# Kernel tuning notes

Hardware: AMD Instinct MI355X
Metric: run time of the kernel (lower is better)

Reference implementation:

```python
import jax, jax.numpy as jnp
import numpy as np

B, S, D = 8, 2048, 256
H, DFF, L = 8, 1024, 5
DK = D // H
EPS = 1e-5


def _xavier(key, shape):
    fan_in, fan_out = shape[-2], shape[-1]
    a = jnp.sqrt(6.0 / (fan_in + fan_out))
    return jax.random.uniform(key, shape, jnp.float32, -a, a)


def setup_inputs() -> dict:
    key = jax.random.key(0)
    ks = jax.random.split(key, 12)
    inp = {
        "src": jax.random.normal(ks[0], (B, S, D), jnp.float32),
        "sph": jax.random.normal(ks[1], (B, S, S), jnp.float32),
        # stacked per-layer parameters, leading dim = L
        "Wq": _xavier(ks[2], (L, D, D)), "bq": jnp.zeros((L, D), jnp.float32),
        "Wk": _xavier(ks[3], (L, D, D)), "bk": jnp.zeros((L, D), jnp.float32),
        "Wv": _xavier(ks[4], (L, D, D)), "bv": jnp.zeros((L, D), jnp.float32),
        "Wo": _xavier(ks[5], (L, D, D)), "bo": jnp.zeros((L, D), jnp.float32),
        "W1": _xavier(ks[6], (L, D, DFF)), "b1": jnp.zeros((L, DFF), jnp.float32),
        "W2": _xavier(ks[7], (L, DFF, D)), "b2": jnp.zeros((L, D), jnp.float32),
        "ln1_g": jnp.ones((L, D), jnp.float32), "ln1_b": jnp.zeros((L, D), jnp.float32),
        "ln2_g": jnp.ones((L, D), jnp.float32), "ln2_b": jnp.zeros((L, D), jnp.float32),
    }
    return inp


def _layernorm(x, g, b):
    mu = jnp.mean(x, axis=-1, keepdims=True)
    var = jnp.mean(jnp.square(x - mu), axis=-1, keepdims=True)
    return (x - mu) * jax.lax.rsqrt(var + EPS) * g + b


def _layer(x, sph, Wq, bq, Wk, bk, Wv, bv, Wo, bo, W1, b1, W2, b2, g1, be1, g2, be2):
    # multihead attention with additive sph score bias
    q = (x @ Wq + bq).reshape(B, S, H, DK)
    k = (x @ Wk + bk).reshape(B, S, H, DK)
    v = (x @ Wv + bv).reshape(B, S, H, DK)
    scores = jnp.einsum("bqhd,bkhd->bhqk", q, k) / jnp.sqrt(jnp.float32(DK))
    scores = scores + sph[:, None, :, :]  # bias broadcast over heads
    attn = jax.nn.softmax(scores, axis=-1)
    ctx = jnp.einsum("bhqk,bkhd->bqhd", attn, v).reshape(B, S, D)
    src2 = ctx @ Wo + bo
    x = _layernorm(x + src2, g1, be1)
    # FFN (exact gelu, matching torch F.gelu default)
    h = jax.nn.gelu(x @ W1 + b1, approximate=False)
    src2 = h @ W2 + b2
    x = _layernorm(x + src2, g2, be2)
    return x


def reference(src, sph, Wq, bq, Wk, bk, Wv, bv, Wo, bo, W1, b1, W2, b2, ln1_g, ln1_b, ln2_g, ln2_b):
    x = src
    for i in range(L):
        x = _layer(x, sph, Wq[i], bq[i], Wk[i], bk[i], Wv[i], bv[i], Wo[i], bo[i],
                   W1[i], b1[i], W2[i], b2[i], ln1_g[i], ln1_b[i], ln2_g[i], ln2_b[i])
    return x
```

## Files before the change

### kernel.cpp

```cpp
#include <hip/hip_runtime.h>
#include <cstdint>

__device__ __forceinline__ float b2f(unsigned short u) {
    unsigned int t = ((unsigned int)u) << 16;
    float f;
    __builtin_memcpy(&f, &t, 4);
    return f;
}
__device__ __forceinline__ unsigned short f2b(float f) {
    unsigned int u;
    __builtin_memcpy(&u, &f, 4);
    unsigned int r = (u + 0x7FFFu + ((u >> 16) & 1u)) >> 16;
    return (unsigned short)r;
}
__device__ __forceinline__ float2 bpair(unsigned int u) {
    float2 r;
    unsigned int lo = u << 16;
    unsigned int hi = u & 0xFFFF0000u;
    __builtin_memcpy(&r.x, &lo, 4);
    __builtin_memcpy(&r.y, &hi, 4);
    return r;
}

typedef __attribute__((ext_vector_type(8))) short bf16x8;
typedef __attribute__((ext_vector_type(4))) float f32x4;

#define LOG2E 1.4426950408889634f
#define SC2   0.2550348595f

__global__ void transcvt_k(const float* __restrict__ in,
                           unsigned short* __restrict__ out, int R, int C,
                           int in_z, int out_z) {
    __shared__ float tile[32][33];
    in += (size_t)blockIdx.z * in_z;
    out += (size_t)blockIdx.z * out_z;
    const int c0 = blockIdx.x * 32, r0 = blockIdx.y * 32;
    const int tx = threadIdx.x, ty = threadIdx.y;
#pragma unroll
    for (int i = 0; i < 32; i += 8)
        tile[ty + i][tx] = in[(size_t)(r0 + ty + i) * C + c0 + tx];
    __syncthreads();
#pragma unroll
    for (int i = 0; i < 32; i += 8)
        out[(size_t)(c0 + ty + i) * R + r0 + tx] = f2b(tile[tx][ty + i]);
}

__global__ __launch_bounds__(256) void sph_cvt(const float* __restrict__ in,
                                               unsigned short* __restrict__ out) {
    const size_t idx = (size_t)blockIdx.x * 256 + threadIdx.x;
    const float4 a = ((const float4*)in)[idx * 2];
    const float4 b = ((const float4*)in)[idx * 2 + 1];
    uint4 o;
    o.x = (unsigned)f2b(a.x * LOG2E) | ((unsigned)f2b(a.y * LOG2E) << 16);
    o.y = (unsigned)f2b(a.z * LOG2E) | ((unsigned)f2b(a.w * LOG2E) << 16);
    o.z = (unsigned)f2b(b.x * LOG2E) | ((unsigned)f2b(b.y * LOG2E) << 16);
    o.w = (unsigned)f2b(b.z * LOG2E) | ((unsigned)f2b(b.w * LOG2E) << 16);
    ((uint4*)out)[idx] = o;
}

template <int AF32, int QKVB>
__global__ __launch_bounds__(256) void gemm_bias_kernel(
    const void* __restrict__ Ap, const unsigned short* __restrict__ Wt,
    const float* __restrict__ biasQ, const float* __restrict__ biasK,
    const float* __restrict__ biasV, unsigned short* __restrict__ C,
    int M, int N, int K, int do_gelu) {
    __shared__ unsigned short As[64 * 40];
    __shared__ unsigned short Bs[64 * 40];
    const int tid = threadIdx.x;
    const int lane = tid & 63, wid = tid >> 6;
    const int m0 = blockIdx.y * 64, n0 = blockIdx.x * 64;
    const int wm = (wid >> 1) * 32, wn = (wid & 1) * 32;
    const int quad = lane >> 4, mrow = lane & 15;
    f32x4 acc[2][2] = {};
    const int arow = tid >> 2, ak = (tid & 3) << 3;
    const unsigned short* Bg = Wt + (size_t)(n0 + arow) * K + ak;
    const float* Agf = (const float*)Ap + (size_t)(m0 + arow) * K + ak;
    const unsigned short* Agb = (const unsigned short*)Ap + (size_t)(m0 + arow) * K + ak;

    typedef __attribute__((ext_vector_type(8))) short short8;
    for (int kb = 0; kb < K; kb += 32) {
        if (AF32) {
            float4 f0 = *(const float4*)(Agf + kb);
            float4 f1 = *(const float4*)(Agf + kb + 4);
            short8 t;
            t[0] = (short)f2b(f0.x); t[1] = (short)f2b(f0.y);
            t[2] = (short)f2b(f0.z); t[3] = (short)f2b(f0.w);
            t[4] = (short)f2b(f1.x); t[5] = (short)f2b(f1.y);
            t[6] = (short)f2b(f1.z); t[7] = (short)f2b(f1.w);
            *(short8*)&As[arow * 40 + ak] = t;
        } else {
            *(uint4*)&As[arow * 40 + ak] = *(const uint4*)(Agb + kb);
        }
        *(uint4*)&Bs[arow * 40 + ak] = *(const uint4*)(Bg + kb);
        __syncthreads();
        bf16x8 a0 = *(const bf16x8*)&As[(wm + mrow) * 40 + quad * 8];
        bf16x8 a1 = *(const bf16x8*)&As[(wm + 16 + mrow) * 40 + quad * 8];
        bf16x8 b0 = *(const bf16x8*)&Bs[(wn + mrow) * 40 + quad * 8];
        bf16x8 b1 = *(const bf16x8*)&Bs[(wn + 16 + mrow) * 40 + quad * 8];
        acc[0][0] = __builtin_amdgcn_mfma_f32_16x16x32_bf16(a0, b0, acc[0][0], 0, 0, 0);
        acc[0][1] = __builtin_amdgcn_mfma_f32_16x16x32_bf16(a0, b1, acc[0][1], 0, 0, 0);
        acc[1][0] = __builtin_amdgcn_mfma_f32_16x16x32_bf16(a1, b0, acc[1][0], 0, 0, 0);
        acc[1][1] = __builtin_amdgcn_mfma_f32_16x16x32_bf16(a1, b1, acc[1][1], 0, 0, 0);
        __syncthreads();
    }
    const float* bp;
    if (QKVB) {
        const int bsel = n0 >> 8;
        bp = bsel == 0 ? biasQ : (bsel == 1 ? biasK : biasV);
    } else {
        bp = biasQ;
    }
#pragma unroll
    for (int i = 0; i < 2; i++)
#pragma unroll
        for (int j = 0; j < 2; j++) {
            const int col = n0 + wn + j * 16 + mrow;
            const float bv = QKVB ? bp[col & 255] : bp[col];
#pragma unroll
            for (int r = 0; r < 4; r++) {
                const int row = m0 + wm + i * 16 + quad * 4 + r;
                float v = acc[i][j][r] + bv;
                if (do_gelu) v = 0.5f * v * (1.0f + erff(v * 0.70710678118654752f));
                C[(size_t)row * N + col] = f2b(v);
            }
        }
}

template <int SPHB16>
__global__ __launch_bounds__(256) void attn_mfma(
    const unsigned short* __restrict__ Qb, const unsigned short* __restrict__ Kb,
    const unsigned short* __restrict__ Vb, const float* __restrict__ sphf,
    const unsigned short* __restrict__ sphb, unsigned short* __restrict__ Ctx) {
    __shared__ unsigned short Ks[64 * 40];
    __shared__ unsigned short Vt[32 * 72];
    __shared__ unsigned short Ps[4][16 * 72];

    const int tid = threadIdx.x, lane = tid & 63, wid = tid >> 6;
    const int quad = lane >> 4, lq = lane & 15;
    const int bid = blockIdx.x;
    const int h = bid >> 8, b = (bid >> 5) & 7, qt = bid & 31;
    const int q0 = qt * 64;
    const size_t bS = (size_t)b * 2048;

    const int skey = tid >> 2, sdg = (tid & 3) << 3;
    const unsigned short* kgp = Kb + (bS + skey) * 768 + h * 32 + sdg;
    const int vkp = tid & 31, vdg = (tid >> 5) << 2;
    const unsigned short* vgp = Vb + (bS + 2 * vkp) * 768 + h * 32 + vdg;

    const bf16x8 qf = *(const bf16x8*)(Qb + (bS + q0 + wid * 16 + lq) * 768 + h * 32 + quad * 8);

    const size_t sprow = ((size_t)b * 2048 + q0 + wid * 16 + quad * 4) * 2048 + lq;
    const float* spf = sphf + sprow;
    const unsigned short* spb = sphb + sprow;

    float l_r[4] = {0.f, 0.f, 0.f, 0.f};
    f32x4 o0 = {}, o1 = {};

    for (int kt = 0; kt < 32; ++kt) {
        const int k0 = kt * 64;
        __syncthreads();
        *(uint4*)&Ks[skey * 40 + sdg] = *(const uint4*)(kgp + (size_t)k0 * 768);
        {
            uint2 va = *(const uint2*)(vgp + (size_t)k0 * 768);
            uint2 vb2 = *(const uint2*)(vgp + (size_t)k0 * 768 + 768);
            *(unsigned int*)&Vt[(vdg + 0) * 72 + 2 * vkp] = (va.x & 0xFFFFu) | (vb2.x << 16);
            *(unsigned int*)&Vt[(vdg + 1) * 72 + 2 * vkp] = (va.x >> 16) | (vb2.x & 0xFFFF0000u);
            *(unsigned int*)&Vt[(vdg + 2) * 72 + 2 * vkp] = (va.y & 0xFFFFu) | (vb2.y << 16);
            *(unsigned int*)&Vt[(vdg + 3) * 72 + 2 * vkp] = (va.y >> 16) | (vb2.y & 0xFFFF0000u);
        }
        __syncthreads();

        const f32x4 zf = {};
        f32x4 sa0 = __builtin_amdgcn_mfma_f32_16x16x32_bf16(
            qf, *(const bf16x8*)&Ks[(0  + lq) * 40 + quad * 8], zf, 0, 0, 0);
        f32x4 sa1 = __builtin_amdgcn_mfma_f32_16x16x32_bf16(
            qf, *(const bf16x8*)&Ks[(16 + lq) * 40 + quad * 8], zf, 0, 0, 0);
        f32x4 sa2 = __builtin_amdgcn_mfma_f32_16x16x32_bf16(
            qf, *(const bf16x8*)&Ks[(32 + lq) * 40 + quad * 8], zf, 0, 0, 0);
        f32x4 sa3 = __builtin_amdgcn_mfma_f32_16x16x32_bf16(
            qf, *(const bf16x8*)&Ks[(48 + lq) * 40 + quad * 8], zf, 0, 0, 0);

#pragma unroll
        for (int r = 0; r < 4; ++r) {
            float sb0, sb1, sb2, sb3;
            if (SPHB16) {
                const unsigned short* spr = spb + (size_t)r * 2048 + k0;
                sb0 = b2f(spr[0]);  sb1 = b2f(spr[16]);
                sb2 = b2f(spr[32]); sb3 = b2f(spr[48]);
            } else {
                const float* spr = spf + (size_t)r * 2048 + k0;
                sb0 = spr[0]  * LOG2E; sb1 = spr[16] * LOG2E;
                sb2 = spr[32] * LOG2E; sb3 = spr[48] * LOG2E;
            }
            const float p0 = __builtin_amdgcn_exp2f(fmaf(sa0[r], SC2, sb0));
            const float p1 = __builtin_amdgcn_exp2f(fmaf(sa1[r], SC2, sb1));
            const float p2 = __builtin_amdgcn_exp2f(fmaf(sa2[r], SC2, sb2));
            const float p3 = __builtin_amdgcn_exp2f(fmaf(sa3[r], SC2, sb3));
            l_r[r] += (p0 + p1) + (p2 + p3);
            unsigned short* pw = &Ps[wid][(quad * 4 + r) * 72 + lq];
            pw[0]  = f2b(p0);
            pw[16] = f2b(p1);
            pw[32] = f2b(p2);
            pw[48] = f2b(p3);
        }

#pragma unroll
        for (int k2 = 0; k2 < 2; ++k2) {
            bf16x8 pf = *(const bf16x8*)&Ps[wid][lq * 72 + k2 * 32 + quad * 8];
            o0 = __builtin_amdgcn_mfma_f32_16x16x32_bf16(
                pf, *(const bf16x8*)&Vt[(0  + lq) * 72 + k2 * 32 + quad * 8], o0, 0, 0, 0);
            o1 = __builtin_amdgcn_mfma_f32_16x16x32_bf16(
                pf, *(const bf16x8*)&Vt[(16 + lq) * 72 + k2 * 32 + quad * 8], o1, 0, 0, 0);
        }
    }

    unsigned short* op = Ctx + (bS + q0 + wid * 16 + quad * 4) * 256 + h * 32;
#pragma unroll
    for (int r = 0; r < 4; ++r) {
        float l = l_r[r];
        l += __shfl_xor(l, 1);
        l += __shfl_xor(l, 2);
        l += __shfl_xor(l, 4);
        l += __shfl_xor(l, 8);
        const float inv = 1.f / l;
        op[r * 256 + lq]      = f2b(o0[r] * inv);
        op[r * 256 + 16 + lq] = f2b(o1[r] * inv);
    }
}

__global__ __launch_bounds__(256) void add_ln_kernel(
    const float* __restrict__ x, const unsigned short* __restrict__ r,
    const float* __restrict__ g, const float* __restrict__ be,
    float* __restrict__ out) {
    const int lane = threadIdx.x & 63, wid = threadIdx.x >> 6;
    const size_t row = (size_t)blockIdx.x * 4 + wid;
    float4 xv = *(const float4*)(x + row * 256 + lane * 4);
    uint2 ru = *(const uint2*)(r + row * 256 + lane * 4);
    float2 ra = bpair(ru.x), rb = bpair(ru.y);
    float v[4] = {xv.x + ra.x, xv.y + ra.y, xv.z + rb.x, xv.w + rb.y};
    float sum = v[0] + v[1] + v[2] + v[3];
#pragma unroll
    for (int off = 32; off; off >>= 1) sum += __shfl_xor(sum, off);
    const float mu = sum * (1.f / 256.f);
    float sq = 0.f;
#pragma unroll
    for (int i = 0; i < 4; i++) { float d = v[i] - mu; sq += d * d; }
#pragma unroll
    for (int off = 32; off; off >>= 1) sq += __shfl_xor(sq, off);
    const float rs = rsqrtf(sq * (1.f / 256.f) + 1e-5f);
    float4 o;
    o.x = (v[0] - mu) * rs * g[lane * 4 + 0] + be[lane * 4 + 0];
    o.y = (v[1] - mu) * rs * g[lane * 4 + 1] + be[lane * 4 + 1];
    o.z = (v[2] - mu) * rs * g[lane * 4 + 2] + be[lane * 4 + 2];
    o.w = (v[3] - mu) * rs * g[lane * 4 + 3] + be[lane * 4 + 3];
    *(float4*)(out + row * 256 + lane * 4) = o;
}

extern "C" void kernel_launch(void* const* d_in, const int* in_sizes, int n_in,
                              void* d_out, int out_size, void* d_ws, size_t ws_size,
                              hipStream_t stream) {
    const float* src = (const float*)d_in[0];
    const float* sph = (const float*)d_in[1];
    const float* Wq  = (const float*)d_in[2];
    const float* bq  = (const float*)d_in[3];
    const float* Wk  = (const float*)d_in[4];
    const float* bk  = (const float*)d_in[5];
    const float* Wv  = (const float*)d_in[6];
    const float* bv  = (const float*)d_in[7];
    const float* Wo  = (const float*)d_in[8];
    const float* bo  = (const float*)d_in[9];
    const float* W1  = (const float*)d_in[10];
    const float* b1  = (const float*)d_in[11];
    const float* W2  = (const float*)d_in[12];
    const float* b2  = (const float*)d_in[13];
    const float* g1  = (const float*)d_in[14];
    const float* be1 = (const float*)d_in[15];
    const float* g2  = (const float*)d_in[16];
    const float* be2 = (const float*)d_in[17];

    char* ws = (char*)d_ws;
    float* X = (float*)d_out;
    unsigned short* QKV = (unsigned short*)(ws + 0);
    unsigned short* CTX = (unsigned short*)(ws + 25165824);
    unsigned short* T2  = (unsigned short*)(ws + 33554432);
    unsigned short* H   = QKV;
    unsigned short* WtQKV = (unsigned short*)(ws + 41943040);
    unsigned short* WtO   = (unsigned short*)(ws + 43909120);
    unsigned short* Wt1   = (unsigned short*)(ws + 44564480);
    unsigned short* Wt2   = (unsigned short*)(ws + 47185920);
    unsigned short* SPHB  = (unsigned short*)(ws + 50331648);
    const int use_b16 = (ws_size >= (size_t)117440512);

    const dim3 tb(32, 8);
    transcvt_k<<<dim3(8, 8, 5),  tb, 0, stream>>>(Wq, WtQKV,          256, 256, 65536, 196608);
    transcvt_k<<<dim3(8, 8, 5),  tb, 0, stream>>>(Wk, WtQKV + 65536,  256, 256, 65536, 196608);
    transcvt_k<<<dim3(8, 8, 5),  tb, 0, stream>>>(Wv, WtQKV + 131072, 256, 256, 65536, 196608);
    transcvt_k<<<dim3(8, 8, 5),  tb, 0, stream>>>(Wo, WtO,            256, 256, 65536, 65536);
    transcvt_k<<<dim3(32, 8, 5), tb, 0, stream>>>(W1, Wt1,            256, 1024, 262144, 262144);
    transcvt_k<<<dim3(8, 32, 5), tb, 0, stream>>>(W2, Wt2,            1024, 256, 262144, 262144);
    if (use_b16) sph_cvt<<<16384, 256, 0, stream>>>(sph, SPHB);

    hipMemcpyAsync(X, src, 16777216, hipMemcpyDeviceToDevice, stream);

    const int M = 16384;
    for (int lyr = 0; lyr < 5; ++lyr) {
        gemm_bias_kernel<1, 1><<<dim3(12, 256), 256, 0, stream>>>(
            X, WtQKV + lyr * 196608, bq + lyr * 256, bk + lyr * 256, bv + lyr * 256,
            QKV, M, 768, 256, 0);
        if (use_b16)
            attn_mfma<1><<<2048, 256, 0, stream>>>(QKV, QKV + 256, QKV + 512, sph, SPHB, CTX);
        else
            attn_mfma<0><<<2048, 256, 0, stream>>>(QKV, QKV + 256, QKV + 512, sph, SPHB, CTX);
        gemm_bias_kernel<0, 0><<<dim3(4, 256), 256, 0, stream>>>(
            CTX, WtO + lyr * 65536, bo + lyr * 256, nullptr, nullptr, T2, M, 256, 256, 0);
        add_ln_kernel<<<4096, 256, 0, stream>>>(X, T2, g1 + lyr * 256, be1 + lyr * 256, X);
        gemm_bias_kernel<1, 0><<<dim3(16, 256), 256, 0, stream>>>(
            X, Wt1 + lyr * 262144, b1 + lyr * 1024, nullptr, nullptr, H, M, 1024, 256, 1);
        gemm_bias_kernel<0, 0><<<dim3(4, 256), 256, 0, stream>>>(
            H, Wt2 + lyr * 262144, b2 + lyr * 256, nullptr, nullptr, T2, M, 256, 1024, 0);
        add_ln_kernel<<<4096, 256, 0, stream>>>(X, T2, g2 + lyr * 256, be2 + lyr * 256, X);
    }
}
```

Baseline: 1.540 ms.

## Keep attention probabilities in registers by transposing score MFMA and permuting V layout

The score MFMA operands are swapped so each lane holds four consecutive keys for one query. The probabilities are then packed with v_cvt_pk_bf16_f32 straight into the A-operand of the PV MFMA, which removes the per-wave LDS P buffer and its store/load round trip. V rows are written to LDS in a permuted key order so they match the register-resident P layout. Bias loads become vectorized float4/uint2 reads, and the row-sum reduction is reworked to match the new lane mapping. The cost is a more fragile layout mapping whose correctness depends on the MFMA register permutation being exactly right.

```diff
diff --git a/kernel.cpp b/kernel.cpp
--- a/kernel.cpp
+++ b/kernel.cpp
@@ -21,9 +21,20 @@
     __builtin_memcpy(&r.y, &hi, 4);
     return r;
 }
+__device__ __forceinline__ unsigned int cvtpk(float lo, float hi) {
+    unsigned int r;
+    asm("v_cvt_pk_bf16_f32 %0, %1, %2" : "=v"(r) : "v"(lo), "v"(hi));
+    return r;
+}
 
 typedef __attribute__((ext_vector_type(8))) short bf16x8;
 typedef __attribute__((ext_vector_type(4))) float f32x4;
+
+__device__ __forceinline__ bf16x8 pack4(unsigned a, unsigned b, unsigned c, unsigned d) {
+    union { uint4 u; bf16x8 v; } x;
+    x.u = (uint4){a, b, c, d};
+    return x.v;
+}
 
 #define LOG2E 1.4426950408889634f
 #define SC2   0.2550348595f
@@ -133,7 +144,6 @@
     const unsigned short* __restrict__ sphb, unsigned short* __restrict__ Ctx) {
     __shared__ unsigned short Ks[64 * 40];
     __shared__ unsigned short Vt[32 * 72];
-    __shared__ unsigned short Ps[4][16 * 72];
 
     const int tid = threadIdx.x, lane = tid & 63, wid = tid >> 6;
     const int quad = lane >> 4, lq = lane & 15;
@@ -146,15 +156,18 @@
     const unsigned short* kgp = Kb + (bS + skey) * 768 + h * 32 + sdg;
     const int vkp = tid & 31, vdg = (tid >> 5) << 2;
     const unsigned short* vgp = Vb + (bS + 2 * vkp) * 768 + h * 32 + vdg;
+    const int vk2 = 2 * vkp;
+    const int vslot = (vk2 & 0x23) | ((vk2 & 0x0C) << 1) | ((vk2 & 0x10) >> 2);
 
     const bf16x8 qf = *(const bf16x8*)(Qb + (bS + q0 + wid * 16 + lq) * 768 + h * 32 + quad * 8);
 
-    const size_t sprow = ((size_t)b * 2048 + q0 + wid * 16 + quad * 4) * 2048 + lq;
-    const float* spf = sphf + sprow;
-    const unsigned short* spb = sphb + sprow;
-
-    float l_r[4] = {0.f, 0.f, 0.f, 0.f};
+    const size_t sbase = ((size_t)b * 2048 + q0 + wid * 16 + lq) * 2048 + 4 * quad;
+    const float* spf_ = sphf + sbase;
+    const unsigned short* spb_ = sphb + sbase;
+
+    float l_lane = 0.f;
     f32x4 o0 = {}, o1 = {};
+    const f32x4 zf = {};
 
     for (int kt = 0; kt < 32; ++kt) {
         const int k0 = kt * 64;
@@ -163,68 +176,58 @@
         {
             uint2 va = *(const uint2*)(vgp + (size_t)k0 * 768);
             uint2 vb2 = *(const uint2*)(vgp + (size_t)k0 * 768 + 768);
-            *(unsigned int*)&Vt[(vdg + 0) * 72 + 2 * vkp] = (va.x & 0xFFFFu) | (vb2.x << 16);
-            *(unsigned int*)&Vt[(vdg + 1) * 72 + 2 * vkp] = (va.x >> 16) | (vb2.x & 0xFFFF0000u);
-            *(unsigned int*)&Vt[(vdg + 2) * 72 + 2 * vkp] = (va.y & 0xFFFFu) | (vb2.y << 16);
-            *(unsigned int*)&Vt[(vdg + 3) * 72 + 2 * vkp] = (va.y >> 16) | (vb2.y & 0xFFFF0000u);
+            *(unsigned int*)&Vt[(vdg + 0) * 72 + vslot] = (va.x & 0xFFFFu) | (vb2.x << 16);
+            *(unsigned int*)&Vt[(vdg + 1) * 72 + vslot] = (va.x >> 16) | (vb2.x & 0xFFFF0000u);
+            *(unsigned int*)&Vt[(vdg + 2) * 72 + vslot] = (va.y & 0xFFFFu) | (vb2.y << 16);
+            *(unsigned int*)&Vt[(vdg + 3) * 72 + vslot] = (va.y >> 16) | (vb2.y & 0xFFFF0000u);
         }
         __syncthreads();
 
-        const f32x4 zf = {};
-        f32x4 sa0 = __builtin_amdgcn_mfma_f32_16x16x32_bf16(
-            qf, *(const bf16x8*)&Ks[(0  + lq) * 40 + quad * 8], zf, 0, 0, 0);
-        f32x4 sa1 = __builtin_amdgcn_mfma_f32_16x16x32_bf16(
-            qf, *(const bf16x8*)&Ks[(16 + lq) * 40 + quad * 8], zf, 0, 0, 0);
-        f32x4 sa2 = __builtin_amdgcn_mfma_f32_16x16x32_bf16(
-            qf, *(const bf16x8*)&Ks[(32 + lq) * 40 + quad * 8], zf, 0, 0, 0);
-        f32x4 sa3 = __builtin_amdgcn_mfma_f32_16x16x32_bf16(
-            qf, *(const bf16x8*)&Ks[(48 + lq) * 40 + quad * 8], zf, 0, 0, 0);
-
-#pragma unroll
-        for (int r = 0; r < 4; ++r) {
+        unsigned int w[4][2];
+#pragma unroll
+        for (int g = 0; g < 4; ++g) {
+            const bf16x8 kf = *(const bf16x8*)&Ks[(16 * g + lq) * 40 + quad * 8];
+            const f32x4 s = __builtin_amdgcn_mfma_f32_16x16x32_bf16(kf, qf, zf, 0, 0, 0);
             float sb0, sb1, sb2, sb3;
             if (SPHB16) {
-                const unsigned short* spr = spb + (size_t)r * 2048 + k0;
-                sb0 = b2f(spr[0]);  sb1 = b2f(spr[16]);
-                sb2 = b2f(spr[32]); sb3 = b2f(spr[48]);
+                const uint2 su = *(const uint2*)(spb_ + k0 + 16 * g);
+                const float2 lo = bpair(su.x), hi = bpair(su.y);
+                sb0 = lo.x; sb1 = lo.y; sb2 = hi.x; sb3 = hi.y;
             } else {
-                const float* spr = spf + (size_t)r * 2048 + k0;
-                sb0 = spr[0]  * LOG2E; sb1 = spr[16] * LOG2E;
-                sb2 = spr[32] * LOG2E; sb3 = spr[48] * LOG2E;
+                const float4 sf = *(const float4*)(spf_ + k0 + 16 * g);
+                sb0 = sf.x * LOG2E; sb1 = sf.y * LOG2E;
+                sb2 = sf.z * LOG2E; sb3 = sf.w * LOG2E;
             }
-            const float p0 = __builtin_amdgcn_exp2f(fmaf(sa0[r], SC2, sb0));
-            const float p1 = __builtin_amdgcn_exp2f(fmaf(sa1[r], SC2, sb1));
-            const float p2 = __builtin_amdgcn_exp2f(fmaf(sa2[r], SC2, sb2));
-            const float p3 = __builtin_amdgcn_exp2f(fmaf(sa3[r], SC2, sb3));
-            l_r[r] += (p0 + p1) + (p2 + p3);
-            unsigned short* pw = &Ps[wid][(quad * 4 + r) * 72 + lq];
-            pw[0]  = f2b(p0);
-            pw[16] = f2b(p1);
-            pw[32] = f2b(p2);
-            pw[48] = f2b(p3);
+            const float p0 = __builtin_amdgcn_exp2f(fmaf(s[0], SC2, sb0));
+            const float p1 = __builtin_amdgcn_exp2f(fmaf(s[1], SC2, sb1));
+            const float p2 = __builtin_amdgcn_exp2f(fmaf(s[2], SC2, sb2));
+            const float p3 = __builtin_amdgcn_exp2f(fmaf(s[3], SC2, sb3));
+            l_lane += (p0 + p1) + (p2 + p3);
+            w[g][0] = cvtpk(p0, p1);
+            w[g][1] = cvtpk(p2, p3);
         }
 
-#pragma unroll
-        for (int k2 = 0; k2 < 2; ++k2) {
-            bf16x8 pf = *(const bf16x8*)&Ps[wid][lq * 72 + k2 * 32 + quad * 8];
-            o0 = __builtin_amdgcn_mfma_f32_16x16x32_bf16(
-                pf, *(const bf16x8*)&Vt[(0  + lq) * 72 + k2 * 32 + quad * 8], o0, 0, 0, 0);
-            o1 = __builtin_amdgcn_mfma_f32_16x16x32_bf16(
-                pf, *(const bf16x8*)&Vt[(16 + lq) * 72 + k2 * 32 + quad * 8], o1, 0, 0, 0);
-        }
-    }
-
+        const bf16x8 pf0 = pack4(w[0][0], w[0][1], w[1][0], w[1][1]);
+        const bf16x8 pf1 = pack4(w[2][0], w[2][1], w[3][0], w[3][1]);
+        o0 = __builtin_amdgcn_mfma_f32_16x16x32_bf16(
+            pf0, *(const bf16x8*)&Vt[(0  + lq) * 72 + 0 * 32 + quad * 8], o0, 0, 0, 0);
+        o1 = __builtin_amdgcn_mfma_f32_16x16x32_bf16(
+            pf0, *(const bf16x8*)&Vt[(16 + lq) * 72 + 0 * 32 + quad * 8], o1, 0, 0, 0);
+        o0 = __builtin_amdgcn_mfma_f32_16x16x32_bf16(
+            pf1, *(const bf16x8*)&Vt[(0  + lq) * 72 + 1 * 32 + quad * 8], o0, 0, 0, 0);
+        o1 = __builtin_amdgcn_mfma_f32_16x16x32_bf16(
+            pf1, *(const bf16x8*)&Vt[(16 + lq) * 72 + 1 * 32 + quad * 8], o1, 0, 0, 0);
+    }
+
+    l_lane += __shfl_xor(l_lane, 16);
+    l_lane += __shfl_xor(l_lane, 32);
+    const float inv = 1.f / l_lane;
     unsigned short* op = Ctx + (bS + q0 + wid * 16 + quad * 4) * 256 + h * 32;
 #pragma unroll
     for (int r = 0; r < 4; ++r) {
-        float l = l_r[r];
-        l += __shfl_xor(l, 1);
-        l += __shfl_xor(l, 2);
-        l += __shfl_xor(l, 4);
-        l += __shfl_xor(l, 8);
-        const float inv = 1.f / l;
-        op[r * 256 + lq]      = f2b(o0[r] * inv);
-        op[r * 256 + 16 + lq] = f2b(o1[r] * inv);
+        const float ir = __shfl(inv, quad * 4 + r);
+        op[r * 256 + lq]      = f2b(o0[r] * ir);
+        op[r * 256 + 16 + lq] = f2b(o1[r] * ir);
     }
 }
 
```

Measured after the change: 1.786 ms. +16.0%, slower.

## Use 128-row GEMM tiles and emit bf16 activations from layernorm

Applied to the files above, without the earlier changes.

Adds a GEMM kernel with 128xTN block tiles, so each warp computes a 64-row slab with more MFMAs per shared-memory load. The layernorm kernel now also writes a bf16 copy of its output, so the QKV and FFN1 GEMMs read bf16 directly instead of converting fp32 activations inside the GEMM. The new path needs a larger workspace and falls back to the old kernels otherwise. Fewer blocks and more accumulator registers per thread may lower occupancy.

```diff
diff --git a/kernel.cpp b/kernel.cpp
--- a/kernel.cpp
+++ b/kernel.cpp
@@ -55,6 +55,19 @@
     o.y = (unsigned)f2b(a.z * LOG2E) | ((unsigned)f2b(a.w * LOG2E) << 16);
     o.z = (unsigned)f2b(b.x * LOG2E) | ((unsigned)f2b(b.y * LOG2E) << 16);
     o.w = (unsigned)f2b(b.z * LOG2E) | ((unsigned)f2b(b.w * LOG2E) << 16);
+    ((uint4*)out)[idx] = o;
+}
+
+__global__ __launch_bounds__(256) void cvt_bf16_k(const float* __restrict__ in,
+                                                  unsigned short* __restrict__ out) {
+    const size_t idx = (size_t)blockIdx.x * 256 + threadIdx.x;
+    const float4 a = ((const float4*)in)[idx * 2];
+    const float4 b = ((const float4*)in)[idx * 2 + 1];
+    uint4 o;
+    o.x = (unsigned)f2b(a.x) | ((unsigned)f2b(a.y) << 16);
+    o.y = (unsigned)f2b(a.z) | ((unsigned)f2b(a.w) << 16);
+    o.z = (unsigned)f2b(b.x) | ((unsigned)f2b(b.y) << 16);
+    o.w = (unsigned)f2b(b.z) | ((unsigned)f2b(b.w) << 16);
     ((uint4*)out)[idx] = o;
 }
 
@@ -114,6 +127,74 @@
     for (int i = 0; i < 2; i++)
 #pragma unroll
         for (int j = 0; j < 2; j++) {
+            const int col = n0 + wn + j * 16 + mrow;
+            const float bv = QKVB ? bp[col & 255] : bp[col];
+#pragma unroll
+            for (int r = 0; r < 4; r++) {
+                const int row = m0 + wm + i * 16 + quad * 4 + r;
+                float v = acc[i][j][r] + bv;
+                if (do_gelu) v = 0.5f * v * (1.0f + erff(v * 0.70710678118654752f));
+                C[(size_t)row * N + col] = f2b(v);
+            }
+        }
+}
+
+template <int TN, int QKVB>
+__global__ __launch_bounds__(256) void gemm128_kernel(
+    const unsigned short* __restrict__ A, const unsigned short* __restrict__ Wt,
+    const float* __restrict__ biasQ, const float* __restrict__ biasK,
+    const float* __restrict__ biasV, unsigned short* __restrict__ C,
+    int M, int N, int K, int do_gelu) {
+    constexpr int JN = TN / 32;
+    __shared__ unsigned short As[128 * 40];
+    __shared__ unsigned short Bs[TN * 40];
+    const int tid = threadIdx.x;
+    const int lane = tid & 63, wid = tid >> 6;
+    const int m0 = blockIdx.y * 128, n0 = blockIdx.x * TN;
+    const int wm = (wid >> 1) * 64, wn = (wid & 1) * (TN / 2);
+    const int quad = lane >> 4, mrow = lane & 15;
+    f32x4 acc[4][JN] = {};
+    const int srow = tid >> 2, scol = (tid & 3) << 3;
+    const unsigned short* Ag = A + (size_t)(m0 + srow) * K + scol;
+    const unsigned short* Bg = Wt + (size_t)(n0 + srow) * K + scol;
+
+    for (int kb = 0; kb < K; kb += 32) {
+        const uint4 a0 = *(const uint4*)(Ag + kb);
+        const uint4 a1 = *(const uint4*)(Ag + (size_t)64 * K + kb);
+        const uint4 b0 = *(const uint4*)(Bg + kb);
+        uint4 b1 = {};
+        if constexpr (TN == 128) b1 = *(const uint4*)(Bg + (size_t)64 * K + kb);
+        __syncthreads();
+        *(uint4*)&As[srow * 40 + scol] = a0;
+        *(uint4*)&As[(srow + 64) * 40 + scol] = a1;
+        *(uint4*)&Bs[srow * 40 + scol] = b0;
+        if constexpr (TN == 128) *(uint4*)&Bs[(srow + 64) * 40 + scol] = b1;
+        __syncthreads();
+        bf16x8 af[4], bfr[JN];
+#pragma unroll
+        for (int i = 0; i < 4; i++)
+            af[i] = *(const bf16x8*)&As[(wm + i * 16 + mrow) * 40 + quad * 8];
+#pragma unroll
+        for (int j = 0; j < JN; j++)
+            bfr[j] = *(const bf16x8*)&Bs[(wn + j * 16 + mrow) * 40 + quad * 8];
+#pragma unroll
+        for (int i = 0; i < 4; i++)
+#pragma unroll
+            for (int j = 0; j < JN; j++)
+                acc[i][j] = __builtin_amdgcn_mfma_f32_16x16x32_bf16(af[i], bfr[j], acc[i][j], 0, 0, 0);
+    }
+
+    const float* bp;
+    if (QKVB) {
+        const int bsel = n0 >> 8;
+        bp = bsel == 0 ? biasQ : (bsel == 1 ? biasK : biasV);
+    } else {
+        bp = biasQ;
+    }
+#pragma unroll
+    for (int i = 0; i < 4; i++)
+#pragma unroll
+        for (int j = 0; j < JN; j++) {
             const int col = n0 + wn + j * 16 + mrow;
             const float bv = QKVB ? bp[col & 255] : bp[col];
 #pragma unroll
@@ -231,7 +312,7 @@
 __global__ __launch_bounds__(256) void add_ln_kernel(
     const float* __restrict__ x, const unsigned short* __restrict__ r,
     const float* __restrict__ g, const float* __restrict__ be,
-    float* __restrict__ out) {
+    float* __restrict__ out, unsigned short* __restrict__ xb) {
     const int lane = threadIdx.x & 63, wid = threadIdx.x >> 6;
     const size_t row = (size_t)blockIdx.x * 4 + wid;
     float4 xv = *(const float4*)(x + row * 256 + lane * 4);
@@ -254,6 +335,12 @@
     o.z = (v[2] - mu) * rs * g[lane * 4 + 2] + be[lane * 4 + 2];
     o.w = (v[3] - mu) * rs * g[lane * 4 + 3] + be[lane * 4 + 3];
     *(float4*)(out + row * 256 + lane * 4) = o;
+    if (xb) {
+        uint2 p;
+        p.x = (unsigned)f2b(o.x) | ((unsigned)f2b(o.y) << 16);
+        p.y = (unsigned)f2b(o.z) | ((unsigned)f2b(o.w) << 16);
+        *(uint2*)(xb + row * 256 + lane * 4) = p;
+    }
 }
 
 extern "C" void kernel_launch(void* const* d_in, const int* in_sizes, int n_in,
@@ -289,7 +376,9 @@
     unsigned short* Wt1   = (unsigned short*)(ws + 44564480);
     unsigned short* Wt2   = (unsigned short*)(ws + 47185920);
     unsigned short* SPHB  = (unsigned short*)(ws + 50331648);
+    unsigned short* XB    = (unsigned short*)(ws + 117440512);
     const int use_b16 = (ws_size >= (size_t)117440512);
+    const int use_xb  = (ws_size >= (size_t)125829120);
 
     const dim3 tb(32, 8);
     transcvt_k<<<dim3(8, 8, 5),  tb, 0, stream>>>(Wq, WtQKV,          256, 256, 65536, 196608);
@@ -299,25 +388,45 @@
     transcvt_k<<<dim3(32, 8, 5), tb, 0, stream>>>(W1, Wt1,            256, 1024, 262144, 262144);
     transcvt_k<<<dim3(8, 32, 5), tb, 0, stream>>>(W2, Wt2,            1024, 256, 262144, 262144);
     if (use_b16) sph_cvt<<<16384, 256, 0, stream>>>(sph, SPHB);
+    if (use_xb)  cvt_bf16_k<<<2048, 256, 0, stream>>>(src, XB);
 
     hipMemcpyAsync(X, src, 16777216, hipMemcpyDeviceToDevice, stream);
 
     const int M = 16384;
+    unsigned short* xb_arg = use_xb ? XB : nullptr;
     for (int lyr = 0; lyr < 5; ++lyr) {
-        gemm_bias_kernel<1, 1><<<dim3(12, 256), 256, 0, stream>>>(
-            X, WtQKV + lyr * 196608, bq + lyr * 256, bk + lyr * 256, bv + lyr * 256,
-            QKV, M, 768, 256, 0);
+        if (use_xb) {
+            gemm128_kernel<128, 1><<<dim3(6, 128), 256, 0, stream>>>(
+                XB, WtQKV + lyr * 196608, bq + lyr * 256, bk + lyr * 256, bv + lyr * 256,
+                QKV, M, 768, 256, 0);
+        } else {
+            gemm_bias_kernel<1, 1><<<dim3(12, 256), 256, 0, stream>>>(
+                X, WtQKV + lyr * 196608, bq + lyr * 256, bk + lyr * 256, bv + lyr * 256,
+                QKV, M, 768, 256, 0);
+        }
         if (use_b16)
             attn_mfma<1><<<2048, 256, 0, stream>>>(QKV, QKV + 256, QKV + 512, sph, SPHB, CTX);
         else
             attn_mfma<0><<<2048, 256, 0, stream>>>(QKV, QKV + 256, QKV + 512, sph, SPHB, CTX);
-        gemm_bias_kernel<0, 0><<<dim3(4, 256), 256, 0, stream>>>(
-            CTX, WtO + lyr * 65536, bo + lyr * 256, nullptr, nullptr, T2, M, 256, 256, 0);
-        add_ln_kernel<<<4096, 256, 0, stream>>>(X, T2, g1 + lyr * 256, be1 + lyr * 256, X);
-        gemm_bias_kernel<1, 0><<<dim3(16, 256), 256, 0, stream>>>(
-            X, Wt1 + lyr * 262144, b1 + lyr * 1024, nullptr, nullptr, H, M, 1024, 256, 1);
-        gemm_bias_kernel<0, 0><<<dim3(4, 256), 256, 0, stream>>>(
-            H, Wt2 + lyr * 262144, b2 + lyr * 256, nullptr, nullptr, T2, M, 256, 1024, 0);
-        add_ln_kernel<<<4096, 256, 0, stream>>>(X, T2, g2 + lyr * 256, be2 + lyr * 256, X);
-    }
-}
+        if (use_xb) {
+            gemm128_kernel<64, 0><<<dim3(4, 128), 256, 0, stream>>>(
+                CTX, WtO + lyr * 65536, bo + lyr * 256, nullptr, nullptr, T2, M, 256, 256, 0);
+        } else {
+            gemm_bias_kernel<0, 0><<<dim3(4, 256), 256, 0, stream>>>(
+                CTX, WtO + lyr * 65536, bo + lyr * 256, nullptr, nullptr, T2, M, 256, 256, 0);
+        }
+        add_ln_kernel<<<4096, 256, 0, stream>>>(X, T2, g1 + lyr * 256, be1 + lyr * 256, X, xb_arg);
+        if (use_xb) {
+            gemm128_kernel<128, 0><<<dim3(8, 128), 256, 0, stream>>>(
+                XB, Wt1 + lyr * 262144, b1 + lyr * 1024, nullptr, nullptr, H, M, 1024, 256, 1);
+            gemm128_kernel<64, 0><<<dim3(4, 128), 256, 0, stream>>>(
+                H, Wt2 + lyr * 262144, b2 + lyr * 256, nullptr, nullptr, T2, M, 256, 1024, 0);
+        } else {
+            gemm_bias_kernel<1, 0><<<dim3(16, 256), 256, 0, stream>>>(
+                X, Wt1 + lyr * 262144, b1 + lyr * 1024, nullptr, nullptr, H, M, 1024, 256, 1);
+            gemm_bias_kernel<0, 0><<<dim3(4, 256), 256, 0, stream>>>(
+                H, Wt2 + lyr * 262144, b2 + lyr * 256, nullptr, nullptr, T2, M, 256, 1024, 0);
+        }
+        add_ln_kernel<<<4096, 256, 0, stream>>>(X, T2, g2 + lyr * 256, be2 + lyr * 256, X, xb_arg);
+    }
+}
```

New measurement: 1.540 ms. Within noise of the previous version (-0.0%).

## Use larger swizzled GEMM tiles with direct global-to-LDS loads and bf16 activations

Applied to the files above, without the earlier changes.

Replaces the 64x64, K=32 GEMM with a 128xTN, K=64 tile kernel that loads operands straight into LDS with global_load_lds and an XOR swizzle to avoid bank conflicts. Each wave now issues 4xJN MFMAs per k-half instead of 2x2. LayerNorm now also writes a bf16 copy of the activations, so the GEMMs no longer convert fp32 inputs on the fly. The aim is more data reuse per tile and fewer load instructions. In exchange the kernel uses more registers and LDS, launches fewer blocks, and adds an extra bf16 write in LayerNorm.

```diff
diff --git a/kernel.cpp b/kernel.cpp
--- a/kernel.cpp
+++ b/kernel.cpp
@@ -27,6 +27,12 @@
 
 #define LOG2E 1.4426950408889634f
 #define SC2   0.2550348595f
+
+__device__ __forceinline__ void gload16(const void* g, void* l) {
+    __builtin_amdgcn_global_load_lds(
+        (const __attribute__((address_space(1))) unsigned int*)g,
+        (__attribute__((address_space(3))) unsigned int*)l, 16, 0, 0);
+}
 
 __global__ void transcvt_k(const float* __restrict__ in,
                            unsigned short* __restrict__ out, int R, int C,
@@ -58,51 +64,74 @@
     ((uint4*)out)[idx] = o;
 }
 
-template <int AF32, int QKVB>
-__global__ __launch_bounds__(256) void gemm_bias_kernel(
-    const void* __restrict__ Ap, const unsigned short* __restrict__ Wt,
+__global__ __launch_bounds__(256) void cvt_bf16_k(const float* __restrict__ in,
+                                                  unsigned short* __restrict__ out) {
+    const size_t idx = (size_t)blockIdx.x * 256 + threadIdx.x;
+    const float4 a = ((const float4*)in)[idx * 2];
+    const float4 b = ((const float4*)in)[idx * 2 + 1];
+    uint4 o;
+    o.x = (unsigned)f2b(a.x) | ((unsigned)f2b(a.y) << 16);
+    o.y = (unsigned)f2b(a.z) | ((unsigned)f2b(a.w) << 16);
+    o.z = (unsigned)f2b(b.x) | ((unsigned)f2b(b.y) << 16);
+    o.w = (unsigned)f2b(b.z) | ((unsigned)f2b(b.w) << 16);
+    ((uint4*)out)[idx] = o;
+}
+
+template <int TN, int QKVB>
+__global__ __launch_bounds__(256) void gemm_gl_kernel(
+    const unsigned short* __restrict__ A, const unsigned short* __restrict__ Wt,
     const float* __restrict__ biasQ, const float* __restrict__ biasK,
     const float* __restrict__ biasV, unsigned short* __restrict__ C,
     int M, int N, int K, int do_gelu) {
-    __shared__ unsigned short As[64 * 40];
-    __shared__ unsigned short Bs[64 * 40];
+    constexpr int JN = TN / 32;
+    constexpr int NCH = 16 + TN / 8;
+    __shared__ unsigned short As[128 * 64];
+    __shared__ unsigned short Bs[TN * 64];
     const int tid = threadIdx.x;
     const int lane = tid & 63, wid = tid >> 6;
-    const int m0 = blockIdx.y * 64, n0 = blockIdx.x * 64;
-    const int wm = (wid >> 1) * 32, wn = (wid & 1) * 32;
+    const int m0 = blockIdx.y * 128, n0 = blockIdx.x * TN;
+    const int wm = (wid >> 1) * 64, wn = (wid & 1) * (TN / 2);
     const int quad = lane >> 4, mrow = lane & 15;
-    f32x4 acc[2][2] = {};
-    const int arow = tid >> 2, ak = (tid & 3) << 3;
-    const unsigned short* Bg = Wt + (size_t)(n0 + arow) * K + ak;
-    const float* Agf = (const float*)Ap + (size_t)(m0 + arow) * K + ak;
-    const unsigned short* Agb = (const unsigned short*)Ap + (size_t)(m0 + arow) * K + ak;
-
-    typedef __attribute__((ext_vector_type(8))) short short8;
-    for (int kb = 0; kb < K; kb += 32) {
-        if (AF32) {
-            float4 f0 = *(const float4*)(Agf + kb);
-            float4 f1 = *(const float4*)(Agf + kb + 4);
-            short8 t;
-            t[0] = (short)f2b(f0.x); t[1] = (short)f2b(f0.y);
-            t[2] = (short)f2b(f0.z); t[3] = (short)f2b(f0.w);
-            t[4] = (short)f2b(f1.x); t[5] = (short)f2b(f1.y);
-            t[6] = (short)f2b(f1.z); t[7] = (short)f2b(f1.w);
-            *(short8*)&As[arow * 40 + ak] = t;
-        } else {
-            *(uint4*)&As[arow * 40 + ak] = *(const uint4*)(Agb + kb);
-        }
-        *(uint4*)&Bs[arow * 40 + ak] = *(const uint4*)(Bg + kb);
+    const int lrow = lane >> 3, lslot = lane & 7;
+    f32x4 acc[4][JN] = {};
+
+    for (int kb = 0; kb < K; kb += 64) {
+#pragma unroll
+        for (int cc = 0; cc < NCH / 4; ++cc) {
+            const int c = wid * (NCH / 4) + cc;
+            if (c < 16) {
+                const int row = c * 8 + lrow;
+                const int gcol = ((lslot ^ (row & 7)) << 3) + kb;
+                gload16(A + (size_t)(m0 + row) * K + gcol, &As[c * 512 + lane * 8]);
+            } else {
+                const int row = (c - 16) * 8 + lrow;
+                const int gcol = ((lslot ^ (row & 7)) << 3) + kb;
+                gload16(Wt + (size_t)(n0 + row) * K + gcol, &Bs[(c - 16) * 512 + lane * 8]);
+            }
+        }
         __syncthreads();
-        bf16x8 a0 = *(const bf16x8*)&As[(wm + mrow) * 40 + quad * 8];
-        bf16x8 a1 = *(const bf16x8*)&As[(wm + 16 + mrow) * 40 + quad * 8];
-        bf16x8 b0 = *(const bf16x8*)&Bs[(wn + mrow) * 40 + quad * 8];
-        bf16x8 b1 = *(const bf16x8*)&Bs[(wn + 16 + mrow) * 40 + quad * 8];
-        acc[0][0] = __builtin_amdgcn_mfma_f32_16x16x32_bf16(a0, b0, acc[0][0], 0, 0, 0);
-        acc[0][1] = __builtin_amdgcn_mfma_f32_16x16x32_bf16(a0, b1, acc[0][1], 0, 0, 0);
-        acc[1][0] = __builtin_amdgcn_mfma_f32_16x16x32_bf16(a1, b0, acc[1][0], 0, 0, 0);
-        acc[1][1] = __builtin_amdgcn_mfma_f32_16x16x32_bf16(a1, b1, acc[1][1], 0, 0, 0);
+#pragma unroll
+        for (int h = 0; h < 2; ++h) {
+            bf16x8 af[4], bfr[JN];
+#pragma unroll
+            for (int i = 0; i < 4; i++) {
+                const int ar = wm + i * 16 + mrow;
+                af[i] = *(const bf16x8*)&As[ar * 64 + (((h * 4 + quad) ^ (ar & 7)) << 3)];
+            }
+#pragma unroll
+            for (int j = 0; j < JN; j++) {
+                const int br = wn + j * 16 + mrow;
+                bfr[j] = *(const bf16x8*)&Bs[br * 64 + (((h * 4 + quad) ^ (br & 7)) << 3)];
+            }
+#pragma unroll
+            for (int i = 0; i < 4; i++)
+#pragma unroll
+                for (int j = 0; j < JN; j++)
+                    acc[i][j] = __builtin_amdgcn_mfma_f32_16x16x32_bf16(af[i], bfr[j], acc[i][j], 0, 0, 0);
+        }
         __syncthreads();
     }
+
     const float* bp;
     if (QKVB) {
         const int bsel = n0 >> 8;
@@ -111,9 +140,9 @@
         bp = biasQ;
     }
 #pragma unroll
-    for (int i = 0; i < 2; i++)
-#pragma unroll
-        for (int j = 0; j < 2; j++) {
+    for (int i = 0; i < 4; i++)
+#pragma unroll
+        for (int j = 0; j < JN; j++) {
             const int col = n0 + wn + j * 16 + mrow;
             const float bv = QKVB ? bp[col & 255] : bp[col];
 #pragma unroll
@@ -229,9 +258,9 @@
 }
 
 __global__ __launch_bounds__(256) void add_ln_kernel(
-    const float* __restrict__ x, const unsigned short* __restrict__ r,
+    const float* x, const unsigned short* r,
     const float* __restrict__ g, const float* __restrict__ be,
-    float* __restrict__ out) {
+    float* out, unsigned short* xb) {
     const int lane = threadIdx.x & 63, wid = threadIdx.x >> 6;
     const size_t row = (size_t)blockIdx.x * 4 + wid;
     float4 xv = *(const float4*)(x + row * 256 + lane * 4);
@@ -254,6 +283,10 @@
     o.z = (v[2] - mu) * rs * g[lane * 4 + 2] + be[lane * 4 + 2];
     o.w = (v[3] - mu) * rs * g[lane * 4 + 3] + be[lane * 4 + 3];
     *(float4*)(out + row * 256 + lane * 4) = o;
+    uint2 p;
+    p.x = (unsigned)f2b(o.x) | ((unsigned)f2b(o.y) << 16);
+    p.y = (unsigned)f2b(o.z) | ((unsigned)f2b(o.w) << 16);
+    *(uint2*)(xb + row * 256 + lane * 4) = p;
 }
 
 extern "C" void kernel_launch(void* const* d_in, const int* in_sizes, int n_in,
@@ -284,6 +317,7 @@
     unsigned short* CTX = (unsigned short*)(ws + 25165824);
     unsigned short* T2  = (unsigned short*)(ws + 33554432);
     unsigned short* H   = QKV;
+    unsigned short* XB  = T2;
     unsigned short* WtQKV = (unsigned short*)(ws + 41943040);
     unsigned short* WtO   = (unsigned short*)(ws + 43909120);
     unsigned short* Wt1   = (unsigned short*)(ws + 44564480);
@@ -299,25 +333,26 @@
     transcvt_k<<<dim3(32, 8, 5), tb, 0, stream>>>(W1, Wt1,            256, 1024, 262144, 262144);
     transcvt_k<<<dim3(8, 32, 5), tb, 0, stream>>>(W2, Wt2,            1024, 256, 262144, 262144);
     if (use_b16) sph_cvt<<<16384, 256, 0, stream>>>(sph, SPHB);
+    cvt_bf16_k<<<2048, 256, 0, stream>>>(src, XB);
 
     hipMemcpyAsync(X, src, 16777216, hipMemcpyDeviceToDevice, stream);
 
     const int M = 16384;
     for (int lyr = 0; lyr < 5; ++lyr) {
-        gemm_bias_kernel<1, 1><<<dim3(12, 256), 256, 0, stream>>>(
-            X, WtQKV + lyr * 196608, bq + lyr * 256, bk + lyr * 256, bv + lyr * 256,
+        gemm_gl_kernel<128, 1><<<dim3(6, 128), 256, 0, stream>>>(
+            XB, WtQKV + lyr * 196608, bq + lyr * 256, bk + lyr * 256, bv + lyr * 256,
             QKV, M, 768, 256, 0);
         if (use_b16)
             attn_mfma<1><<<2048, 256, 0, stream>>>(QKV, QKV + 256, QKV + 512, sph, SPHB, CTX);
         else
             attn_mfma<0><<<2048, 256, 0, stream>>>(QKV, QKV + 256, QKV + 512, sph, SPHB, CTX);
-        gemm_bias_kernel<0, 0><<<dim3(4, 256), 256, 0, stream>>>(
+        gemm_gl_kernel<64, 0><<<dim3(4, 128), 256, 0, stream>>>(
             CTX, WtO + lyr * 65536, bo + lyr * 256, nullptr, nullptr, T2, M, 256, 256, 0);
-        add_ln_kernel<<<4096, 256, 0, stream>>>(X, T2, g1 + lyr * 256, be1 + lyr * 256, X);
-        gemm_bias_kernel<1, 0><<<dim3(16, 256), 256, 0, stream>>>(
-            X, Wt1 + lyr * 262144, b1 + lyr * 1024, nullptr, nullptr, H, M, 1024, 256, 1);
-        gemm_bias_kernel<0, 0><<<dim3(4, 256), 256, 0, stream>>>(
+        add_ln_kernel<<<4096, 256, 0, stream>>>(X, T2, g1 + lyr * 256, be1 + lyr * 256, X, XB);
+        gemm_gl_kernel<128, 0><<<dim3(8, 128), 256, 0, stream>>>(
+            XB, Wt1 + lyr * 262144, b1 + lyr * 1024, nullptr, nullptr, H, M, 1024, 256, 1);
+        gemm_gl_kernel<64, 0><<<dim3(4, 128), 256, 0, stream>>>(
             H, Wt2 + lyr * 262144, b2 + lyr * 256, nullptr, nullptr, T2, M, 256, 1024, 0);
-        add_ln_kernel<<<4096, 256, 0, stream>>>(X, T2, g2 + lyr * 256, be2 + lyr * 256, X);
-    }
-}
+        add_ln_kernel<<<4096, 256, 0, stream>>>(X, T2, g2 + lyr * 256, be2 + lyr * 256, X, XB);
+    }
+}
```

After: 1.493 ms. -3.1%, faster.
